# Kernel optimization log

Hardware: AMD Instinct MI355X
Metric: run time of the kernel (lower is better)

Reference implementation:

```python
import jax, jax.numpy as jnp
import numpy as np

C, T, H = 256, 16, 8
D = C // H  # head dim = 32
SCALE = float((D * T) ** 0.5)


def setup_inputs() -> dict:
    key = jax.random.key(0)
    kx, kk, kq, kv = jax.random.split(key, 4)
    B, P = 8, 1024
    x = jax.random.normal(kx, (B, C, P, T), dtype=jnp.float32)
    # 1x1 conv weights, no bias -> [out_ch, in_ch]
    Wk = jax.random.normal(kk, (C, C), dtype=jnp.float32) * 0.02
    Wq = jax.random.normal(kq, (C, C), dtype=jnp.float32) * 0.02
    Wv = jax.random.normal(kv, (C, C), dtype=jnp.float32) * 0.02
    return {"x": x, "Wk": Wk, "Wq": Wq, "Wv": Wv}


def _proj_split(W, x):
    # 1x1 conv == channel matmul, then split heads: b (h d) p t -> b h d p t
    B, _, P, Tt = x.shape
    y = jnp.einsum('oc,bcpt->bopt', W, x)
    return y.reshape(B, H, D, P, Tt)


def reference(x, Wk, Wq, Wv):
    B, _, P, Tt = x.shape
    k = _proj_split(Wk, x)  # [B,H,D,P,T]
    q = _proj_split(Wq, x)
    v = _proj_split(Wv, x)
    # energy over spatial positions, contracting head-dim and time
    energy = jnp.einsum('bhdpt,bhdqt->bhpq', k, q)  # [B,H,P,P]
    attn = jax.nn.softmax(energy / SCALE, axis=-1)
    out = jnp.einsum('bhpq,bhdpt->bhdqt', attn, v)  # [B,H,D,P,T]
    return out.reshape(B, C, P, Tt)
```

## Files before the change

kernel.cpp:

```cpp
#include <hip/hip_runtime.h>


typedef unsigned char u8;
typedef unsigned short u16;
typedef unsigned int u32;
typedef unsigned long long u64;
typedef __attribute__((ext_vector_type(8))) short bfx8;
typedef __attribute__((ext_vector_type(4))) float fx4;
typedef __attribute__((ext_vector_type(2))) long lx2;

constexpr float KC1 = 1.4426950408889634f / 22.627416997969522f;
constexpr float KC8 = KC1 / 256.0f;
constexpr float S8 = 16.0f;

__device__ __forceinline__ u16 f2bf(float f) {
  u32 u = __builtin_bit_cast(u32, f);
  return (u16)((u + 0x7fffu + ((u >> 16) & 1u)) >> 16);
}
__device__ __forceinline__ float bf2f(u16 v) {
  return __builtin_bit_cast(float, (u32)v << 16);
}
__device__ __forceinline__ fx4 mfma16(bfx8 a, bfx8 b, fx4 c) {
  return __builtin_amdgcn_mfma_f32_16x16x32_bf16(a, b, c, 0, 0, 0);
}
__device__ __forceinline__ fx4 mfma8(long a, long b, fx4 c) {
  return __builtin_amdgcn_mfma_f32_16x16x32_fp8_fp8(a, b, c, 0, 0, 0);
}
typedef __attribute__((address_space(1))) const unsigned int* as1p;
typedef __attribute__((address_space(3))) unsigned int* as3p;
__device__ __forceinline__ void gll16(const void* g, void* l) {
  __builtin_amdgcn_global_load_lds((as1p)g, (as3p)l, 16, 0, 0);
}
#define SB0 __builtin_amdgcn_sched_barrier(0)
#define VMC0 do { asm volatile("s_waitcnt vmcnt(0)" ::: "memory"); SB0; } while (0)

template <bool SWAP, int NT, int LK>
__device__ __forceinline__ void gemmW(const u16* __restrict__ Ag,
                                      const u16* __restrict__ Bg,
                                      u16* lds, fx4 (&acc)[4][4],
                                      int wv, int lane) {
  const int l15 = lane & 15, kg = lane >> 4, l7 = lane & 7;
  const int wr = wv >> 2, wn = wv & 3;
  const int rsub = lane >> 3, csub = (lane & 7) * 8;

  auto stg = [&](const u16* g, int ldsoff, int t) {
#pragma unroll
    for (int i = 0; i < 2; ++i)
      gll16(g + (size_t)(wv * 16 + i * 8 + rsub) * LK + t * 64 + csub,
            lds + ldsoff + (wv * 16 + i * 8) * 64);
  };
  bfx8 af[4], bf[4];
  auto rdA = [&](int kk, int aoff) {
#pragma unroll
    for (int mt = 0; mt < 4; ++mt)
      af[mt] = *(const bfx8*)(lds + aoff + (wr * 64 + mt * 16 + l15) * 64 +
                              (((kk << 2) + kg) ^ l7) * 8);
  };
  auto rdB = [&](int kk, int boff) {
#pragma unroll
    for (int nt = 0; nt < 4; ++nt)
      bf[nt] = *(const bfx8*)(lds + boff + (wn * 64 + nt * 16 + l15) * 64 +
                              (((kk << 2) + kg) ^ l7) * 8);
  };
  auto MM = [&]() {
    __builtin_amdgcn_s_setprio(1);
#pragma unroll
    for (int mt = 0; mt < 4; ++mt)
#pragma unroll
      for (int nt = 0; nt < 4; ++nt) {
        if constexpr (SWAP)
          acc[mt][nt] = mfma16(bf[nt], af[mt], acc[mt][nt]);
        else
          acc[mt][nt] = mfma16(af[mt], bf[nt], acc[mt][nt]);
      }
    __builtin_amdgcn_s_setprio(0);
  };

  stg(Ag, 0, 0); stg(Bg, 32768, 0);
  VMC0;
  __builtin_amdgcn_s_barrier();
  SB0;
#pragma unroll 1
  for (int t = 0; t < NT; ++t) {
    const int cA = (t & 1) ? 16384 : 0, cB = (t & 1) ? 49152 : 32768;
    const int nA = (t & 1) ? 0 : 16384, nB = (t & 1) ? 32768 : 49152;
    const bool more = (t + 1 < NT);
    if (more) { stg(Ag, nA, t + 1); stg(Bg, nB, t + 1); }
    rdA(0, cA); rdB(0, cB);
    MM();
    rdA(1, cA); rdB(1, cB);
    MM();
    if (more) {
      VMC0;
      __builtin_amdgcn_s_barrier();
      SB0;
    }
  }
}

template <int NT, int LK>
__device__ __forceinline__ void gemmWf(const u8* __restrict__ Ag,
                                       const u8* __restrict__ Bg,
                                       u8* lds, fx4 (&acc)[4][4],
                                       int wv, int lane) {
  const int l15 = lane & 15, kg = lane >> 4;
  const int wr = wv >> 2, wn = wv & 3;
  const int rs4 = lane >> 2, c16 = (lane & 3) * 16;
  const int usw = (kg ^ ((l15 >> 1) & 3)) << 4;

  auto stg = [&](const u8* g, int ldsoff, int t) {
    gll16(g + (size_t)(wv * 16 + rs4) * LK + t * 64 + c16, lds + ldsoff + wv * 1024);
  };
  lx2 af[4], bf[4];
  auto rdA = [&](int aoff) {
#pragma unroll
    for (int mt = 0; mt < 4; ++mt)
      af[mt] = *(const lx2*)(lds + aoff + (wr * 64 + mt * 16 + l15) * 64 + usw);
  };
  auto rdB = [&](int boff) {
#pragma unroll
    for (int nt = 0; nt < 4; ++nt)
      bf[nt] = *(const lx2*)(lds + boff + (wn * 64 + nt * 16 + l15) * 64 + usw);
  };
  auto MM = [&](int kk) {
    __builtin_amdgcn_s_setprio(1);
#pragma unroll
    for (int mt = 0; mt < 4; ++mt)
#pragma unroll
      for (int nt = 0; nt < 4; ++nt)
        acc[mt][nt] = mfma8(kk ? bf[nt].y : bf[nt].x,
                            kk ? af[mt].y : af[mt].x, acc[mt][nt]);
    __builtin_amdgcn_s_setprio(0);
  };

  stg(Ag, 0, 0); stg(Bg, 32768, 0);
  VMC0;
  __builtin_amdgcn_s_barrier();
  SB0;
#pragma unroll 1
  for (int t = 0; t < NT; ++t) {
    const int cA = (t & 1) ? 16384 : 0, cB = (t & 1) ? 49152 : 32768;
    const int nA = (t & 1) ? 0 : 16384, nB = (t & 1) ? 32768 : 49152;
    const bool more = (t + 1 < NT);
    if (more) { stg(Ag, nA, t + 1); stg(Bg, nB, t + 1); }
    rdA(cA); rdB(cB);
    MM(0);
    MM(1);
    if (more) {
      VMC0;
      __builtin_amdgcn_s_barrier();
      SB0;
    }
  }
}

__global__ __launch_bounds__(256) void k_wconv(const float* __restrict__ Wk,
                                               const float* __restrict__ Wq,
                                               const float* __restrict__ Wv,
                                               u16* __restrict__ Wall) {
  int blk = blockIdx.x;
  int pr = blk >> 5;
  const float* src = (pr == 0) ? Wk : ((pr == 1) ? Wq : Wv);
  int oc = (blk & 31) * 8 + (threadIdx.x >> 5);
  int Cc = threadIdx.x & 31;
  const float4* s4 = (const float4*)(src + oc * 256 + Cc * 8);
  float4 a = s4[0], b = s4[1];
  alignas(16) u16 t[8] = {f2bf(a.x), f2bf(a.y), f2bf(a.z), f2bf(a.w),
                          f2bf(b.x), f2bf(b.y), f2bf(b.z), f2bf(b.w)};
  int o = pr * 256 + oc;
  int pos = (Cc & ~7) + ((Cc & 7) ^ (o & 7));
  *(uint4*)(Wall + o * 256 + pos * 8) = *(const uint4*)t;
}

__global__ __launch_bounds__(256) void k_xt(const float* __restrict__ x,
                                            u16* __restrict__ Xbf) {
  __shared__ u16 Xs[128 * 256];
  int b = blockIdx.x >> 7;
  int n0 = (blockIdx.x & 127) * 128;
  int tid = threadIdx.x;
  int ng = tid & 31, cgrp = tid >> 5;
  const float* xb = x + (size_t)b * 4194304 + n0 + ng * 4;
#pragma unroll
  for (int it = 0; it < 4; ++it) {
    int Cc = cgrp + it * 8;
    float4 v[8];
#pragma unroll
    for (int i = 0; i < 8; ++i)
      v[i] = *(const float4*)(xb + (size_t)(Cc * 8 + i) * 16384);
#pragma unroll
    for (int j = 0; j < 4; ++j) {
      int n = ng * 4 + j;
      alignas(16) u16 c8v[8];
#pragma unroll
      for (int i = 0; i < 8; ++i) c8v[i] = f2bf(((const float*)&v[i])[j]);
      int pos = (Cc & ~7) + ((Cc & 7) ^ (n & 7));
      *(uint4*)&Xs[n * 256 + pos * 8] = *(const uint4*)c8v;
    }
  }
  __syncthreads();
  u16* xo = Xbf + (size_t)b * 4194304 + (size_t)n0 * 256;
#pragma unroll
  for (int it = 0; it < 16; ++it) {
    int idx = tid + it * 256;
    int n = idx >> 5, chp = idx & 31;
    uint4 v = *(const uint4*)&Xs[n * 256 + chp * 8];
    *(uint4*)&xo[(size_t)n * 256 + chp * 8] = v;
  }
}

__global__ __launch_bounds__(1024, 4) void k_proj2(const u16* __restrict__ Xbf,
                                                   const u16* __restrict__ Wall,
                                                   u8* __restrict__ Kb8, u8* __restrict__ Qb8,
                                                   u16* __restrict__ Vb) {
  __shared__ u16 lds[65536];
  int bid = blockIdx.x;
  int vid = (bid & 7) * 192 + (bid >> 3);
  int nidx = vid / 3;
  int otile = vid - nidx * 3;
  int b = nidx >> 6, ntile = nidx & 63;
  int tid = threadIdx.x, lane = tid & 63, wv = tid >> 6;
  int l15 = lane & 15, kg = lane >> 4;
  int wr = wv >> 2, wn = wv & 3;
  const u16* Ag = Wall + otile * 65536;
  const u16* Bg = Xbf + (size_t)b * 4194304 + (size_t)ntile * 65536;
  fx4 acc[4][4];
#pragma unroll
  for (int mt = 0; mt < 4; ++mt)
#pragma unroll
    for (int nt = 0; nt < 4; ++nt) acc[mt][nt] = (fx4)0.0f;

  gemmW<true, 4, 256>(Ag, Bg, lds, acc, wv, lane);

#pragma unroll
  for (int mt = 0; mt < 4; ++mt) {
    int o = wr * 64 + mt * 16 + l15;
    int h = o >> 5, d = o & 31;
    int f0 = d * 16 + kg * 4;
    if (otile < 2) {
      u8* dst = (otile == 0) ? Kb8 : Qb8;
      size_t bhro = (size_t)(b * 8 + h) * 524288;
      int tk = f0 >> 6, kb = f0 & 63;
      int kkb = kb >> 5, kgl = (kb >> 3) & 3, off = kb & 7;
#pragma unroll
      for (int nt = 0; nt < 4; ++nt) {
        int n = wn * 64 + nt * 16 + kg * 4;
        int p = ntile * 16 + (n >> 4);
        const fx4& a4 = acc[mt][nt];
        u32 w = __builtin_amdgcn_cvt_pk_fp8_f32(a4[0] * S8, a4[1] * S8, 0, false);
        w = __builtin_amdgcn_cvt_pk_fp8_f32(a4[2] * S8, a4[3] * S8, w, true);
        int phys = tk * 64 + ((kgl ^ ((p >> 1) & 3)) << 4) + kkb * 8 + off;
        *(u32*)(dst + bhro + (size_t)p * 512 + phys) = w;
      }
    } else {
      size_t bhro = (size_t)(b * 8 + h) * 524288;
      int f7 = f0 & 7, fc = f0 >> 3;
#pragma unroll
      for (int nt = 0; nt < 4; ++nt) {
        int n = wn * 64 + nt * 16 + kg * 4;
        int p = ntile * 16 + (n >> 4);
        alignas(8) u16 e4[4];
#pragma unroll
        for (int j = 0; j < 4; ++j) e4[j] = f2bf(acc[mt][nt][j]);
        int ch = fc ^ (p & 7);
        *(u64*)(Vb + bhro + (size_t)p * 512 + ch * 8 + f7) = *(const u64*)e4;
      }
    }
  }
}

__global__ __launch_bounds__(1024, 4) void k_egemm(const u8* __restrict__ Qb8,
                                                   const u8* __restrict__ Kb8,
                                                   u16* __restrict__ Pt,
                                                   float* __restrict__ Zpart) {
  __shared__ u8 lds[65536];
  int bid = blockIdx.x;
  int vid = (bid & 7) * 128 + (bid >> 3);
  int bh = vid >> 4, qt = (vid >> 2) & 3, pt = vid & 3;
  int q0 = qt * 256, p0 = pt * 256;
  int tid = threadIdx.x, lane = tid & 63, wv = tid >> 6;
  int l15 = lane & 15, kg = lane >> 4;
  int wr = wv >> 2, wn = wv & 3;
  const u8* Ag = Qb8 + (size_t)bh * 524288 + (size_t)q0 * 512;
  const u8* Bg = Kb8 + (size_t)bh * 524288 + (size_t)p0 * 512;
  fx4 acc[4][4];
#pragma unroll
  for (int mt = 0; mt < 4; ++mt)
#pragma unroll
    for (int nt = 0; nt < 4; ++nt) acc[mt][nt] = (fx4)0.0f;

  gemmWf<8, 512>(Ag, Bg, lds, acc, wv, lane);

  size_t pbase = (size_t)bh * 1048576;
  float zac[4][4];
#pragma unroll
  for (int nt = 0; nt < 4; ++nt)
#pragma unroll
    for (int j = 0; j < 4; ++j) zac[nt][j] = 0.f;
#pragma unroll
  for (int mt = 0; mt < 4; ++mt) {
    int q = q0 + wr * 64 + mt * 16 + l15;
    size_t qrow = pbase + (size_t)q * 1024;
    int q7 = l15 & 7;
#pragma unroll
    for (int nt = 0; nt < 4; ++nt) {
      int p4 = p0 + wn * 64 + nt * 16 + kg * 4;
      alignas(8) u16 e4[4];
#pragma unroll
      for (int j = 0; j < 4; ++j) {
        float e = exp2f(acc[mt][nt][j] * KC8);
        zac[nt][j] += e;
        e4[j] = f2bf(e);
      }
      int ch = (p4 >> 3) ^ q7;
      *(u64*)(Pt + qrow + ch * 8 + (p4 & 7)) = *(const u64*)e4;
    }
  }
#pragma unroll
  for (int nt = 0; nt < 4; ++nt)
#pragma unroll
    for (int j = 0; j < 4; ++j) {
      float v = zac[nt][j];
      v += __shfl_xor(v, 1);
      v += __shfl_xor(v, 2);
      v += __shfl_xor(v, 4);
      v += __shfl_xor(v, 8);
      zac[nt][j] = v;
    }
  if (l15 == 0) {
    size_t zb = (size_t)(qt * 4 + wr) * 65536 + (size_t)bh * 1024;
#pragma unroll
    for (int nt = 0; nt < 4; ++nt) {
      int p4 = p0 + wn * 64 + nt * 16 + kg * 4;
      float4 zv;
      zv.x = zac[nt][0]; zv.y = zac[nt][1];
      zv.z = zac[nt][2]; zv.w = zac[nt][3];
      *(float4*)&Zpart[zb + p4] = zv;
    }
  }
}

__global__ __launch_bounds__(256) void k_zfinal(const float* __restrict__ Zpart,
                                                float* __restrict__ RZ) {
  int idx = blockIdx.x * 256 + threadIdx.x;
  float s = 0.f;
#pragma unroll
  for (int k = 0; k < 16; ++k) s += Zpart[(size_t)k * 65536 + idx];
  RZ[idx] = 1.0f / s;
}

__global__ __launch_bounds__(256) void k_vt(const u16* __restrict__ Vb,
                                            const float* __restrict__ RZ,
                                            u16* __restrict__ Vt) {
  __shared__ u16 Vl[64 * 512];
  int bh = blockIdx.x >> 4;
  int ptile = blockIdx.x & 15;
  int tid = threadIdx.x;
  const u16* src = Vb + (size_t)bh * 524288 + (size_t)ptile * 32768;
#pragma unroll
  for (int it = 0; it < 16; ++it) {
    int idx = tid + it * 256;
    int pl = idx >> 6, g = idx & 63;
    float rz = RZ[bh * 1024 + ptile * 64 + pl];
    uint4 v = *(const uint4*)&src[(size_t)pl * 512 + g * 8];
    int cf = g ^ (pl & 7);
    u32 w[4] = {v.x, v.y, v.z, v.w};
    alignas(16) u16 c8v[8];
#pragma unroll
    for (int i = 0; i < 4; ++i) {
      c8v[2 * i]     = f2bf(bf2f((u16)w[i]) * rz);
      c8v[2 * i + 1] = f2bf(bf2f((u16)(w[i] >> 16)) * rz);
    }
    *(uint4*)&Vl[pl * 512 + cf * 8] = *(const uint4*)c8v;
  }
  __syncthreads();
  u16* dst = Vt + (size_t)bh * 524288;
#pragma unroll
  for (int it = 0; it < 16; ++it) {
    int f = (tid & 63) + (it & 7) * 64;
    int pc = (tid >> 6) * 2 + (it >> 3);
    int base = pc * 8 * 512 + f;
    u32 x0 = (u32)Vl[base] | ((u32)Vl[base + 512] << 16);
    u32 x1 = (u32)Vl[base + 1024] | ((u32)Vl[base + 1536] << 16);
    u32 x2 = (u32)Vl[base + 2048] | ((u32)Vl[base + 2560] << 16);
    u32 x3 = (u32)Vl[base + 3072] | ((u32)Vl[base + 3584] << 16);
    uint4 pk; pk.x = x0; pk.y = x1; pk.z = x2; pk.w = x3;
    int col = ptile * 8 + (pc ^ (f & 7));
    *(uint4*)&dst[(size_t)f * 1024 + col * 8] = pk;
  }
}

__global__ __launch_bounds__(1024, 4) void k_pv(const u16* __restrict__ Pt,
                                                const u16* __restrict__ Vt,
                                                float* __restrict__ out) {
  __shared__ u16 lds[65536];
  int bid = blockIdx.x;
  int vid = (bid & 7) * 64 + (bid >> 3);
  int bh = vid >> 3, tile = vid & 7;
  int q0 = (tile >> 1) * 256, f0 = (tile & 1) * 256;
  int tid = threadIdx.x, lane = tid & 63, wv = tid >> 6;
  int l15 = lane & 15, kg = lane >> 4;
  int wr = wv >> 2, wn = wv & 3;
  const u16* Ag = Pt + (size_t)bh * 1048576 + (size_t)q0 * 1024;
  const u16* Bg = Vt + (size_t)bh * 524288 + (size_t)f0 * 1024;
  fx4 acc[4][4];
#pragma unroll
  for (int mt = 0; mt < 4; ++mt)
#pragma unroll
    for (int nt = 0; nt < 4; ++nt) acc[mt][nt] = (fx4)0.0f;

  gemmW<true, 16, 1024>(Ag, Bg, lds, acc, wv, lane);

#pragma unroll
  for (int mt = 0; mt < 4; ++mt) {
    int q = q0 + wr * 64 + mt * 16 + l15;
#pragma unroll
    for (int nt = 0; nt < 4; ++nt) {
      int fb = f0 + wn * 64 + nt * 16 + kg * 4;
      int d = fb >> 4, t0 = fb & 15;
      float4 v;
      v.x = acc[mt][nt][0];
      v.y = acc[mt][nt][1];
      v.z = acc[mt][nt][2];
      v.w = acc[mt][nt][3];
      *(float4*)&out[(size_t)(bh * 32 + d) * 16384 + (size_t)q * 16 + t0] = v;
    }
  }
}

extern "C" void kernel_launch(void* const* d_in, const int* in_sizes, int n_in,
                              void* d_out, int out_size, void* d_ws, size_t ws_size,
                              hipStream_t stream) {
  (void)in_sizes; (void)n_in; (void)out_size; (void)ws_size;
  const float* x  = (const float*)d_in[0];
  const float* Wk = (const float*)d_in[1];
  const float* Wq = (const float*)d_in[2];
  const float* Wv = (const float*)d_in[3];
  float* out = (float*)d_out;

  u8* base = (u8*)d_ws;
  u8*  Kb8 = base;
  u8*  Qb8 = base + 33554432;
  u16* Vb  = (u16*)(base + 67108864);
  u16* Xbf = (u16*)(base + 134217728);
  u16* Pt  = Xbf;
  u16* Vt  = (u16*)(base + 268435456);
  float* Zpart = (float*)(base + 335544320);
  float* RZ = Zpart + 1048576;
  u16* Wall = (u16*)(RZ + 65536);

  k_wconv<<<96, 256, 0, stream>>>(Wk, Wq, Wv, Wall);
  k_xt<<<1024, 256, 0, stream>>>(x, Xbf);
  k_proj2<<<1536, 1024, 0, stream>>>(Xbf, Wall, Kb8, Qb8, Vb);
  k_egemm<<<1024, 1024, 0, stream>>>(Qb8, Kb8, Pt, Zpart);
  k_zfinal<<<256, 256, 0, stream>>>(Zpart, RZ);
  k_vt<<<1024, 256, 0, stream>>>(Vb, RZ, Vt);
  k_pv<<<512, 1024, 0, stream>>>(Pt, Vt, out);
}
```

Before: 322.2 us.

## Make egemm and pv blocks loop over multiple output tiles persistently

The GEMM helpers gain a segment loop with a per-segment epilogue callback, so each block computes several consecutive output tiles (4 for the energy GEMM, 2 for PV) that share the same A rows. Grid sizes drop from 1024 to 256 and from 512 to 256, which cuts per-block launch and prologue overhead and may improve L2 reuse of the Q and P tiles. In exchange, the epilogue now runs serially between segments with a pipeline restart, and 256 blocks of 1024 threads may underfill the 256 CUs or leave too little parallelism to hide latency.

```diff
diff --git a/kernel.cpp b/kernel.cpp
--- a/kernel.cpp
+++ b/kernel.cpp
@@ -34,11 +34,11 @@
 #define SB0 __builtin_amdgcn_sched_barrier(0)
 #define VMC0 do { asm volatile("s_waitcnt vmcnt(0)" ::: "memory"); SB0; } while (0)
 
-template <bool SWAP, int NT, int LK>
-__device__ __forceinline__ void gemmW(const u16* __restrict__ Ag,
-                                      const u16* __restrict__ Bg,
-                                      u16* lds, fx4 (&acc)[4][4],
-                                      int wv, int lane) {
+template <bool SWAP, int NSEG, int NT, int LK, int ASEG, int BSEG, typename Epi>
+__device__ __forceinline__ void gemmWM(const u16* __restrict__ Ag,
+                                       const u16* __restrict__ Bg,
+                                       u16* lds, fx4 (&acc)[4][4],
+                                       int wv, int lane, Epi&& epi) {
   const int l15 = lane & 15, kg = lane >> 4, l7 = lane & 7;
   const int wr = wv >> 2, wn = wv & 3;
   const int rsub = lane >> 3, csub = (lane & 7) * 8;
@@ -81,16 +81,29 @@
   __builtin_amdgcn_s_barrier();
   SB0;
 #pragma unroll 1
-  for (int t = 0; t < NT; ++t) {
-    const int cA = (t & 1) ? 16384 : 0, cB = (t & 1) ? 49152 : 32768;
-    const int nA = (t & 1) ? 0 : 16384, nB = (t & 1) ? 32768 : 49152;
-    const bool more = (t + 1 < NT);
-    if (more) { stg(Ag, nA, t + 1); stg(Bg, nB, t + 1); }
-    rdA(0, cA); rdB(0, cB);
-    MM();
-    rdA(1, cA); rdB(1, cB);
-    MM();
-    if (more) {
+  for (int s = 0; s < NSEG; ++s) {
+    const u16* As_ = Ag + (size_t)s * ASEG;
+    const u16* Bs_ = Bg + (size_t)s * BSEG;
+#pragma unroll 1
+    for (int t = 0; t < NT; ++t) {
+      const int cA = (t & 1) ? 16384 : 0, cB = (t & 1) ? 49152 : 32768;
+      const int nA = (t & 1) ? 0 : 16384, nB = (t & 1) ? 32768 : 49152;
+      const bool more = (t + 1 < NT);
+      if (more) { stg(As_, nA, t + 1); stg(Bs_, nB, t + 1); }
+      rdA(0, cA); rdB(0, cB);
+      MM();
+      rdA(1, cA); rdB(1, cB);
+      MM();
+      if (more) {
+        VMC0;
+        __builtin_amdgcn_s_barrier();
+        SB0;
+      }
+    }
+    epi(s);
+    if (s + 1 < NSEG) {
+      stg(Ag + (size_t)(s + 1) * ASEG, 0, 0);
+      stg(Bg + (size_t)(s + 1) * BSEG, 32768, 0);
       VMC0;
       __builtin_amdgcn_s_barrier();
       SB0;
@@ -98,11 +111,11 @@
   }
 }
 
-template <int NT, int LK>
-__device__ __forceinline__ void gemmWf(const u8* __restrict__ Ag,
-                                       const u8* __restrict__ Bg,
-                                       u8* lds, fx4 (&acc)[4][4],
-                                       int wv, int lane) {
+template <int NSEG, int NT, int LK, int ASEG, int BSEG, typename Epi>
+__device__ __forceinline__ void gemmWfM(const u8* __restrict__ Ag,
+                                        const u8* __restrict__ Bg,
+                                        u8* lds, fx4 (&acc)[4][4],
+                                        int wv, int lane, Epi&& epi) {
   const int l15 = lane & 15, kg = lane >> 4;
   const int wr = wv >> 2, wn = wv & 3;
   const int rs4 = lane >> 2, c16 = (lane & 3) * 16;
@@ -138,15 +151,28 @@
   __builtin_amdgcn_s_barrier();
   SB0;
 #pragma unroll 1
-  for (int t = 0; t < NT; ++t) {
-    const int cA = (t & 1) ? 16384 : 0, cB = (t & 1) ? 49152 : 32768;
-    const int nA = (t & 1) ? 0 : 16384, nB = (t & 1) ? 32768 : 49152;
-    const bool more = (t + 1 < NT);
-    if (more) { stg(Ag, nA, t + 1); stg(Bg, nB, t + 1); }
-    rdA(cA); rdB(cB);
-    MM(0);
-    MM(1);
-    if (more) {
+  for (int s = 0; s < NSEG; ++s) {
+    const u8* As_ = Ag + (size_t)s * ASEG;
+    const u8* Bs_ = Bg + (size_t)s * BSEG;
+#pragma unroll 1
+    for (int t = 0; t < NT; ++t) {
+      const int cA = (t & 1) ? 16384 : 0, cB = (t & 1) ? 49152 : 32768;
+      const int nA = (t & 1) ? 0 : 16384, nB = (t & 1) ? 32768 : 49152;
+      const bool more = (t + 1 < NT);
+      if (more) { stg(As_, nA, t + 1); stg(Bs_, nB, t + 1); }
+      rdA(cA); rdB(cB);
+      MM(0);
+      MM(1);
+      if (more) {
+        VMC0;
+        __builtin_amdgcn_s_barrier();
+        SB0;
+      }
+    }
+    epi(s);
+    if (s + 1 < NSEG) {
+      stg(Ag + (size_t)(s + 1) * ASEG, 0, 0);
+      stg(Bg + (size_t)(s + 1) * BSEG, 32768, 0);
       VMC0;
       __builtin_amdgcn_s_barrier();
       SB0;
@@ -229,43 +255,45 @@
 #pragma unroll
     for (int nt = 0; nt < 4; ++nt) acc[mt][nt] = (fx4)0.0f;
 
-  gemmW<true, 4, 256>(Ag, Bg, lds, acc, wv, lane);
-
-#pragma unroll
-  for (int mt = 0; mt < 4; ++mt) {
-    int o = wr * 64 + mt * 16 + l15;
-    int h = o >> 5, d = o & 31;
-    int f0 = d * 16 + kg * 4;
-    if (otile < 2) {
-      u8* dst = (otile == 0) ? Kb8 : Qb8;
-      size_t bhro = (size_t)(b * 8 + h) * 524288;
-      int tk = f0 >> 6, kb = f0 & 63;
-      int kkb = kb >> 5, kgl = (kb >> 3) & 3, off = kb & 7;
-#pragma unroll
-      for (int nt = 0; nt < 4; ++nt) {
-        int n = wn * 64 + nt * 16 + kg * 4;
-        int p = ntile * 16 + (n >> 4);
-        const fx4& a4 = acc[mt][nt];
-        u32 w = __builtin_amdgcn_cvt_pk_fp8_f32(a4[0] * S8, a4[1] * S8, 0, false);
-        w = __builtin_amdgcn_cvt_pk_fp8_f32(a4[2] * S8, a4[3] * S8, w, true);
-        int phys = tk * 64 + ((kgl ^ ((p >> 1) & 3)) << 4) + kkb * 8 + off;
-        *(u32*)(dst + bhro + (size_t)p * 512 + phys) = w;
-      }
-    } else {
-      size_t bhro = (size_t)(b * 8 + h) * 524288;
-      int f7 = f0 & 7, fc = f0 >> 3;
-#pragma unroll
-      for (int nt = 0; nt < 4; ++nt) {
-        int n = wn * 64 + nt * 16 + kg * 4;
-        int p = ntile * 16 + (n >> 4);
-        alignas(8) u16 e4[4];
-#pragma unroll
-        for (int j = 0; j < 4; ++j) e4[j] = f2bf(acc[mt][nt][j]);
-        int ch = fc ^ (p & 7);
-        *(u64*)(Vb + bhro + (size_t)p * 512 + ch * 8 + f7) = *(const u64*)e4;
-      }
-    }
-  }
+  auto epi = [&](int) {
+#pragma unroll
+    for (int mt = 0; mt < 4; ++mt) {
+      int o = wr * 64 + mt * 16 + l15;
+      int h = o >> 5, d = o & 31;
+      int f0 = d * 16 + kg * 4;
+      if (otile < 2) {
+        u8* dst = (otile == 0) ? Kb8 : Qb8;
+        size_t bhro = (size_t)(b * 8 + h) * 524288;
+        int tk = f0 >> 6, kb = f0 & 63;
+        int kkb = kb >> 5, kgl = (kb >> 3) & 3, off = kb & 7;
+#pragma unroll
+        for (int nt = 0; nt < 4; ++nt) {
+          int n = wn * 64 + nt * 16 + kg * 4;
+          int p = ntile * 16 + (n >> 4);
+          const fx4& a4 = acc[mt][nt];
+          u32 w = __builtin_amdgcn_cvt_pk_fp8_f32(a4[0] * S8, a4[1] * S8, 0, false);
+          w = __builtin_amdgcn_cvt_pk_fp8_f32(a4[2] * S8, a4[3] * S8, w, true);
+          int phys = tk * 64 + ((kgl ^ ((p >> 1) & 3)) << 4) + kkb * 8 + off;
+          *(u32*)(dst + bhro + (size_t)p * 512 + phys) = w;
+        }
+      } else {
+        size_t bhro = (size_t)(b * 8 + h) * 524288;
+        int f7 = f0 & 7, fc = f0 >> 3;
+#pragma unroll
+        for (int nt = 0; nt < 4; ++nt) {
+          int n = wn * 64 + nt * 16 + kg * 4;
+          int p = ntile * 16 + (n >> 4);
+          alignas(8) u16 e4[4];
+#pragma unroll
+          for (int j = 0; j < 4; ++j) e4[j] = f2bf(acc[mt][nt][j]);
+          int ch = fc ^ (p & 7);
+          *(u64*)(Vb + bhro + (size_t)p * 512 + ch * 8 + f7) = *(const u64*)e4;
+        }
+      }
+    }
+  };
+
+  gemmWM<true, 1, 4, 256, 0, 0>(Ag, Bg, lds, acc, wv, lane, epi);
 }
 
 __global__ __launch_bounds__(1024, 4) void k_egemm(const u8* __restrict__ Qb8,
@@ -274,69 +302,73 @@
                                                    float* __restrict__ Zpart) {
   __shared__ u8 lds[65536];
   int bid = blockIdx.x;
-  int vid = (bid & 7) * 128 + (bid >> 3);
-  int bh = vid >> 4, qt = (vid >> 2) & 3, pt = vid & 3;
-  int q0 = qt * 256, p0 = pt * 256;
+  int vid = (bid & 7) * 32 + (bid >> 3);
+  int bh = vid >> 2, qt = vid & 3;
+  int q0 = qt * 256;
   int tid = threadIdx.x, lane = tid & 63, wv = tid >> 6;
   int l15 = lane & 15, kg = lane >> 4;
   int wr = wv >> 2, wn = wv & 3;
   const u8* Ag = Qb8 + (size_t)bh * 524288 + (size_t)q0 * 512;
-  const u8* Bg = Kb8 + (size_t)bh * 524288 + (size_t)p0 * 512;
+  const u8* Bg = Kb8 + (size_t)bh * 524288;
+  size_t pbase = (size_t)bh * 1048576;
   fx4 acc[4][4];
 #pragma unroll
   for (int mt = 0; mt < 4; ++mt)
 #pragma unroll
     for (int nt = 0; nt < 4; ++nt) acc[mt][nt] = (fx4)0.0f;
 
-  gemmWf<8, 512>(Ag, Bg, lds, acc, wv, lane);
-
-  size_t pbase = (size_t)bh * 1048576;
-  float zac[4][4];
-#pragma unroll
-  for (int nt = 0; nt < 4; ++nt)
-#pragma unroll
-    for (int j = 0; j < 4; ++j) zac[nt][j] = 0.f;
-#pragma unroll
-  for (int mt = 0; mt < 4; ++mt) {
-    int q = q0 + wr * 64 + mt * 16 + l15;
-    size_t qrow = pbase + (size_t)q * 1024;
-    int q7 = l15 & 7;
-#pragma unroll
-    for (int nt = 0; nt < 4; ++nt) {
-      int p4 = p0 + wn * 64 + nt * 16 + kg * 4;
-      alignas(8) u16 e4[4];
+  auto epi = [&](int s) {
+    int p0 = s * 256;
+    float zac[4][4];
+#pragma unroll
+    for (int nt = 0; nt < 4; ++nt)
+#pragma unroll
+      for (int j = 0; j < 4; ++j) zac[nt][j] = 0.f;
+#pragma unroll
+    for (int mt = 0; mt < 4; ++mt) {
+      int q = q0 + wr * 64 + mt * 16 + l15;
+      size_t qrow = pbase + (size_t)q * 1024;
+      int q7 = l15 & 7;
+#pragma unroll
+      for (int nt = 0; nt < 4; ++nt) {
+        int p4 = p0 + wn * 64 + nt * 16 + kg * 4;
+        alignas(8) u16 e4[4];
+#pragma unroll
+        for (int j = 0; j < 4; ++j) {
+          float e = exp2f(acc[mt][nt][j] * KC8);
+          zac[nt][j] += e;
+          e4[j] = f2bf(e);
+        }
+        int ch = (p4 >> 3) ^ q7;
+        *(u64*)(Pt + qrow + ch * 8 + (p4 & 7)) = *(const u64*)e4;
+        acc[mt][nt] = (fx4)0.0f;
+      }
+    }
+#pragma unroll
+    for (int nt = 0; nt < 4; ++nt)
 #pragma unroll
       for (int j = 0; j < 4; ++j) {
-        float e = exp2f(acc[mt][nt][j] * KC8);
-        zac[nt][j] += e;
-        e4[j] = f2bf(e);
-      }
-      int ch = (p4 >> 3) ^ q7;
-      *(u64*)(Pt + qrow + ch * 8 + (p4 & 7)) = *(const u64*)e4;
-    }
-  }
-#pragma unroll
-  for (int nt = 0; nt < 4; ++nt)
-#pragma unroll
-    for (int j = 0; j < 4; ++j) {
-      float v = zac[nt][j];
-      v += __shfl_xor(v, 1);
-      v += __shfl_xor(v, 2);
-      v += __shfl_xor(v, 4);
-      v += __shfl_xor(v, 8);
-      zac[nt][j] = v;
-    }
-  if (l15 == 0) {
-    size_t zb = (size_t)(qt * 4 + wr) * 65536 + (size_t)bh * 1024;
-#pragma unroll
-    for (int nt = 0; nt < 4; ++nt) {
-      int p4 = p0 + wn * 64 + nt * 16 + kg * 4;
-      float4 zv;
-      zv.x = zac[nt][0]; zv.y = zac[nt][1];
-      zv.z = zac[nt][2]; zv.w = zac[nt][3];
-      *(float4*)&Zpart[zb + p4] = zv;
-    }
-  }
+        float v = zac[nt][j];
+        v += __shfl_xor(v, 1);
+        v += __shfl_xor(v, 2);
+        v += __shfl_xor(v, 4);
+        v += __shfl_xor(v, 8);
+        zac[nt][j] = v;
+      }
+    if (l15 == 0) {
+      size_t zb = (size_t)(qt * 4 + wr) * 65536 + (size_t)bh * 1024;
+#pragma unroll
+      for (int nt = 0; nt < 4; ++nt) {
+        int p4 = p0 + wn * 64 + nt * 16 + kg * 4;
+        float4 zv;
+        zv.x = zac[nt][0]; zv.y = zac[nt][1];
+        zv.z = zac[nt][2]; zv.w = zac[nt][3];
+        *(float4*)&Zpart[zb + p4] = zv;
+      }
+    }
+  };
+
+  gemmWfM<4, 8, 512, 0, 131072>(Ag, Bg, lds, acc, wv, lane, epi);
 }
 
 __global__ __launch_bounds__(256) void k_zfinal(const float* __restrict__ Zpart,
@@ -394,37 +426,41 @@
                                                 float* __restrict__ out) {
   __shared__ u16 lds[65536];
   int bid = blockIdx.x;
-  int vid = (bid & 7) * 64 + (bid >> 3);
-  int bh = vid >> 3, tile = vid & 7;
-  int q0 = (tile >> 1) * 256, f0 = (tile & 1) * 256;
+  int vid = (bid & 7) * 32 + (bid >> 3);
+  int bh = vid >> 2, qt = vid & 3;
+  int q0 = qt * 256;
   int tid = threadIdx.x, lane = tid & 63, wv = tid >> 6;
   int l15 = lane & 15, kg = lane >> 4;
   int wr = wv >> 2, wn = wv & 3;
   const u16* Ag = Pt + (size_t)bh * 1048576 + (size_t)q0 * 1024;
-  const u16* Bg = Vt + (size_t)bh * 524288 + (size_t)f0 * 1024;
+  const u16* Bg = Vt + (size_t)bh * 524288;
   fx4 acc[4][4];
 #pragma unroll
   for (int mt = 0; mt < 4; ++mt)
 #pragma unroll
     for (int nt = 0; nt < 4; ++nt) acc[mt][nt] = (fx4)0.0f;
 
-  gemmW<true, 16, 1024>(Ag, Bg, lds, acc, wv, lane);
-
-#pragma unroll
-  for (int mt = 0; mt < 4; ++mt) {
-    int q = q0 + wr * 64 + mt * 16 + l15;
-#pragma unroll
-    for (int nt = 0; nt < 4; ++nt) {
-      int fb = f0 + wn * 64 + nt * 16 + kg * 4;
-      int d = fb >> 4, t0 = fb & 15;
-      float4 v;
-      v.x = acc[mt][nt][0];
-      v.y = acc[mt][nt][1];
-      v.z = acc[mt][nt][2];
-      v.w = acc[mt][nt][3];
-      *(float4*)&out[(size_t)(bh * 32 + d) * 16384 + (size_t)q * 16 + t0] = v;
-    }
-  }
+  auto epi = [&](int s) {
+    int f0 = s * 256;
+#pragma unroll
+    for (int mt = 0; mt < 4; ++mt) {
+      int q = q0 + wr * 64 + mt * 16 + l15;
+#pragma unroll
+      for (int nt = 0; nt < 4; ++nt) {
+        int fb = f0 + wn * 64 + nt * 16 + kg * 4;
+        int d = fb >> 4, t0 = fb & 15;
+        float4 v;
+        v.x = acc[mt][nt][0];
+        v.y = acc[mt][nt][1];
+        v.z = acc[mt][nt][2];
+        v.w = acc[mt][nt][3];
+        *(float4*)&out[(size_t)(bh * 32 + d) * 16384 + (size_t)q * 16 + t0] = v;
+        acc[mt][nt] = (fx4)0.0f;
+      }
+    }
+  };
+
+  gemmWM<true, 2, 16, 1024, 0, 262144>(Ag, Bg, lds, acc, wv, lane, epi);
 }
 
 extern "C" void kernel_launch(void* const* d_in, const int* in_sizes, int n_in,
@@ -451,8 +487,8 @@
   k_wconv<<<96, 256, 0, stream>>>(Wk, Wq, Wv, Wall);
   k_xt<<<1024, 256, 0, stream>>>(x, Xbf);
   k_proj2<<<1536, 1024, 0, stream>>>(Xbf, Wall, Kb8, Qb8, Vb);
-  k_egemm<<<1024, 1024, 0, stream>>>(Qb8, Kb8, Pt, Zpart);
+  k_egemm<<<256, 1024, 0, stream>>>(Qb8, Kb8, Pt, Zpart);
   k_zfinal<<<256, 256, 0, stream>>>(Zpart, RZ);
   k_vt<<<1024, 256, 0, stream>>>(Vb, RZ, Vt);
-  k_pv<<<512, 1024, 0, stream>>>(Pt, Vt, out);
-}
+  k_pv<<<256, 1024, 0, stream>>>(Pt, Vt, out);
+}
```

After: 332.8 us. 3.3% more time.

## Rewrite PV GEMM as 8-wave pipelined kernel and fold Z-reduction into transpose

Applied to the files above, without the earlier changes.

The P·V GEMM moves from 16-wave blocks to 8-wave blocks with a 256x256 tile per block. Each wave now computes a 2x2 grid of 64x32 sub-tiles and uses a new gemm8 routine that interleaves half-tile global-to-LDS staging with MFMA phases, using partial vmcnt waits and priority bumps. Separately, the softmax denominator reduction (k_zfinal) is folded into k_vt, which removes one kernel launch and the RZ round trip. The costs are more registers per wave, a more intricate barrier schedule, and the reduction now being repeated by each of the 16 ptile blocks, each summing only its own 64 entries.

```diff
diff --git a/kernel.cpp b/kernel.cpp
--- a/kernel.cpp
+++ b/kernel.cpp
@@ -33,6 +33,12 @@
 }
 #define SB0 __builtin_amdgcn_sched_barrier(0)
 #define VMC0 do { asm volatile("s_waitcnt vmcnt(0)" ::: "memory"); SB0; } while (0)
+#define VMC4 do { asm volatile("s_waitcnt vmcnt(4)" ::: "memory"); SB0; } while (0)
+__device__ __forceinline__ void midbar_() { __builtin_amdgcn_s_barrier(); }
+__device__ __forceinline__ void pend_() {
+  __builtin_amdgcn_s_barrier();
+  SB0;
+}
 
 template <bool SWAP, int NT, int LK>
 __device__ __forceinline__ void gemmW(const u16* __restrict__ Ag,
@@ -154,6 +160,95 @@
   }
 }
 
+template <bool SWAP, int NT, int LK>
+__device__ __forceinline__ void gemm8(const u16* __restrict__ Ag,
+                                      const u16* __restrict__ Bg,
+                                      u16* lds, fx4 (&acc)[2][4][2][2],
+                                      int wv, int lane) {
+  const int l15 = lane & 15, kg = lane >> 4, l7 = lane & 7;
+  const int wr = wv >> 2, wn = wv & 3;
+  const int rsub = lane >> 3, csub = (lane & 7) * 8;
+  constexpr int A0 = 0, A1 = 16384, B0 = 32768, B1 = 49152;
+  bfx8 af[4][2], bf[2][2][2];
+
+  auto stg = [&](const u16* g, int ldsoff, int tile, int half) {
+    const u16* gp = g + (size_t)(half * 128 + wv * 16 + rsub) * LK + tile * 64 + csub;
+    u16* lp = lds + ldsoff + half * 8192 + wv * 1024;
+    gll16(gp, lp);
+    gll16(gp + (size_t)8 * LK, lp + 512);
+  };
+  auto LA = [&](int boff, int mh) {
+    const u16* base = lds + boff + mh * 8192 + wr * 4096;
+#pragma unroll
+    for (int mt = 0; mt < 4; ++mt)
+#pragma unroll
+      for (int kk = 0; kk < 2; ++kk)
+        af[mt][kk] = *(const bfx8*)(base + (mt * 16 + l15) * 64 + (((kk << 2) + kg) ^ l7) * 8);
+  };
+  auto LB = [&](int boff, int nh) {
+    const u16* base = lds + boff + nh * 8192 + wn * 2048;
+#pragma unroll
+    for (int nt = 0; nt < 2; ++nt)
+#pragma unroll
+      for (int kk = 0; kk < 2; ++kk)
+        bf[nh][nt][kk] = *(const bfx8*)(base + (nt * 16 + l15) * 64 + (((kk << 2) + kg) ^ l7) * 8);
+  };
+  auto MM = [&](int mh, int nh) {
+    __builtin_amdgcn_s_setprio(1);
+#pragma unroll
+    for (int mt = 0; mt < 4; ++mt)
+#pragma unroll
+      for (int nt = 0; nt < 2; ++nt)
+#pragma unroll
+        for (int kk = 0; kk < 2; ++kk) {
+          if constexpr (SWAP)
+            acc[mh][mt][nh][nt] = mfma16(bf[nh][nt][kk], af[mt][kk], acc[mh][mt][nh][nt]);
+          else
+            acc[mh][mt][nh][nt] = mfma16(af[mt][kk], bf[nh][nt][kk], acc[mh][mt][nh][nt]);
+        }
+    __builtin_amdgcn_s_setprio(0);
+  };
+
+  stg(Ag, A0, 0, 0); stg(Ag, A0, 0, 1);
+  stg(Bg, B0, 0, 0); stg(Bg, B0, 0, 1);
+  stg(Ag, A1, 1, 0); stg(Bg, B1, 1, 1);
+  VMC4;
+  pend_();
+
+  constexpr int NI = NT / 2;
+#pragma unroll 1
+  for (int i = 0; i < NI; ++i) {
+    const int t = 2 * i;
+    const bool more = (i + 1 < NI);
+    LA(A0, 0); LB(B0, 0);
+    stg(Ag, A1, t + 1, 1);
+    midbar_(); MM(0, 0); pend_();
+    LB(B0, 1);
+    stg(Bg, B1, t + 1, 0);
+    midbar_(); MM(0, 1); pend_();
+    LA(A0, 1);
+    if (more) stg(Ag, A0, t + 2, 0);
+    midbar_(); MM(1, 1); pend_();
+    if (more) stg(Bg, B0, t + 2, 1);
+    midbar_(); MM(1, 0);
+    if (more) { VMC4; } else { VMC0; }
+    pend_();
+    LA(A1, 0); LB(B1, 0);
+    if (more) stg(Ag, A0, t + 2, 1);
+    midbar_(); MM(0, 0); pend_();
+    LB(B1, 1);
+    if (more) stg(Bg, B0, t + 2, 0);
+    midbar_(); MM(0, 1); pend_();
+    LA(A1, 1);
+    if (more) stg(Ag, A1, t + 3, 0);
+    midbar_(); MM(1, 1); pend_();
+    if (more) stg(Bg, B1, t + 3, 1);
+    midbar_(); MM(1, 0);
+    if (more) { VMC4; }
+    pend_();
+  }
+}
+
 __global__ __launch_bounds__(256) void k_wconv(const float* __restrict__ Wk,
                                                const float* __restrict__ Wq,
                                                const float* __restrict__ Wv,
@@ -339,28 +434,28 @@
   }
 }
 
-__global__ __launch_bounds__(256) void k_zfinal(const float* __restrict__ Zpart,
-                                                float* __restrict__ RZ) {
-  int idx = blockIdx.x * 256 + threadIdx.x;
-  float s = 0.f;
-#pragma unroll
-  for (int k = 0; k < 16; ++k) s += Zpart[(size_t)k * 65536 + idx];
-  RZ[idx] = 1.0f / s;
-}
-
 __global__ __launch_bounds__(256) void k_vt(const u16* __restrict__ Vb,
-                                            const float* __restrict__ RZ,
+                                            const float* __restrict__ Zpart,
                                             u16* __restrict__ Vt) {
   __shared__ u16 Vl[64 * 512];
+  __shared__ float rzs[64];
   int bh = blockIdx.x >> 4;
   int ptile = blockIdx.x & 15;
   int tid = threadIdx.x;
+  if (tid < 64) {
+    float s = 0.f;
+#pragma unroll
+    for (int k = 0; k < 16; ++k)
+      s += Zpart[(size_t)k * 65536 + bh * 1024 + ptile * 64 + tid];
+    rzs[tid] = 1.0f / s;
+  }
+  __syncthreads();
   const u16* src = Vb + (size_t)bh * 524288 + (size_t)ptile * 32768;
 #pragma unroll
   for (int it = 0; it < 16; ++it) {
     int idx = tid + it * 256;
     int pl = idx >> 6, g = idx & 63;
-    float rz = RZ[bh * 1024 + ptile * 64 + pl];
+    float rz = rzs[pl];
     uint4 v = *(const uint4*)&src[(size_t)pl * 512 + g * 8];
     int cf = g ^ (pl & 7);
     u32 w[4] = {v.x, v.y, v.z, v.w};
@@ -389,9 +484,9 @@
   }
 }
 
-__global__ __launch_bounds__(1024, 4) void k_pv(const u16* __restrict__ Pt,
-                                                const u16* __restrict__ Vt,
-                                                float* __restrict__ out) {
+__global__ __launch_bounds__(512) void k_pv(const u16* __restrict__ Pt,
+                                            const u16* __restrict__ Vt,
+                                            float* __restrict__ out) {
   __shared__ u16 lds[65536];
   int bid = blockIdx.x;
   int vid = (bid & 7) * 64 + (bid >> 3);
@@ -402,29 +497,37 @@
   int wr = wv >> 2, wn = wv & 3;
   const u16* Ag = Pt + (size_t)bh * 1048576 + (size_t)q0 * 1024;
   const u16* Bg = Vt + (size_t)bh * 524288 + (size_t)f0 * 1024;
-  fx4 acc[4][4];
-#pragma unroll
-  for (int mt = 0; mt < 4; ++mt)
-#pragma unroll
-    for (int nt = 0; nt < 4; ++nt) acc[mt][nt] = (fx4)0.0f;
-
-  gemmW<true, 16, 1024>(Ag, Bg, lds, acc, wv, lane);
-
-#pragma unroll
-  for (int mt = 0; mt < 4; ++mt) {
-    int q = q0 + wr * 64 + mt * 16 + l15;
-#pragma unroll
-    for (int nt = 0; nt < 4; ++nt) {
-      int fb = f0 + wn * 64 + nt * 16 + kg * 4;
-      int d = fb >> 4, t0 = fb & 15;
-      float4 v;
-      v.x = acc[mt][nt][0];
-      v.y = acc[mt][nt][1];
-      v.z = acc[mt][nt][2];
-      v.w = acc[mt][nt][3];
-      *(float4*)&out[(size_t)(bh * 32 + d) * 16384 + (size_t)q * 16 + t0] = v;
-    }
-  }
+  fx4 acc[2][4][2][2];
+#pragma unroll
+  for (int mh = 0; mh < 2; ++mh)
+#pragma unroll
+    for (int mt = 0; mt < 4; ++mt)
+#pragma unroll
+      for (int nh = 0; nh < 2; ++nh)
+#pragma unroll
+        for (int nt = 0; nt < 2; ++nt) acc[mh][mt][nh][nt] = (fx4)0.0f;
+
+  gemm8<true, 16, 1024>(Ag, Bg, lds, acc, wv, lane);
+
+#pragma unroll
+  for (int mh = 0; mh < 2; ++mh)
+#pragma unroll
+    for (int mt = 0; mt < 4; ++mt) {
+      int q = q0 + mh * 128 + wr * 64 + mt * 16 + l15;
+#pragma unroll
+      for (int nh = 0; nh < 2; ++nh)
+#pragma unroll
+        for (int nt = 0; nt < 2; ++nt) {
+          int fb = f0 + nh * 128 + wn * 32 + nt * 16 + kg * 4;
+          int d = fb >> 4, t0 = fb & 15;
+          float4 v;
+          v.x = acc[mh][mt][nh][nt][0];
+          v.y = acc[mh][mt][nh][nt][1];
+          v.z = acc[mh][mt][nh][nt][2];
+          v.w = acc[mh][mt][nh][nt][3];
+          *(float4*)&out[(size_t)(bh * 32 + d) * 16384 + (size_t)q * 16 + t0] = v;
+        }
+    }
 }
 
 extern "C" void kernel_launch(void* const* d_in, const int* in_sizes, int n_in,
@@ -452,7 +555,6 @@
   k_xt<<<1024, 256, 0, stream>>>(x, Xbf);
   k_proj2<<<1536, 1024, 0, stream>>>(Xbf, Wall, Kb8, Qb8, Vb);
   k_egemm<<<1024, 1024, 0, stream>>>(Qb8, Kb8, Pt, Zpart);
-  k_zfinal<<<256, 256, 0, stream>>>(Zpart, RZ);
-  k_vt<<<1024, 256, 0, stream>>>(Vb, RZ, Vt);
-  k_pv<<<512, 1024, 0, stream>>>(Pt, Vt, out);
-}
+  k_vt<<<1024, 256, 0, stream>>>(Vb, Zpart, Vt);
+  k_pv<<<512, 512, 0, stream>>>(Pt, Vt, out);
+}
```

Result: faster. 312.8 us (-2.9%).
